# Performance work log

Measured on AMD Instinct MI355X. Metric: run time of the kernel, lower is better.

The kernel has to match this reference:

```python
import jax, jax.numpy as jnp
import numpy as np


def setup_inputs() -> dict:
    key = jax.random.key(0)
    k1, k2 = jax.random.split(key)
    B, S, F, C = 4, 1024, 512, 4   # batch, time, freq bins, in_filters
    T, K, O = 2, 4, 4              # time half-window, harmonics, out_filters
    x_in = jax.random.normal(k1, (B, S, F, C), dtype=jnp.float32)
    W = jax.random.normal(k2, (2 * T + 1, K, C, O), dtype=jnp.float32) * 0.05
    return {"x_in": x_in, "W": W}


def reference(x_in, W):
    # W: [2T+1, K, C, O]
    T = (W.shape[0] - 1) // 2
    K = W.shape[1]
    B, S, F, C = x_in.shape
    # pad time axis by T on each side (as in tf.pad in the original)
    x_pad = jnp.pad(x_in, ((0, 0), (T, T), (0, 0), (0, 0)))  # [B, S+2T, F, C]
    # harmonic index table: idx[omega, k] = (k+1) * omega, masked when out of band
    k_range = jnp.arange(1, K + 1)                 # [K]
    omega = jnp.arange(F)                          # [F]
    idx = omega[:, None] * k_range[None, :]        # [F, K]
    valid = (idx < F)                              # [F, K]
    idx_c = jnp.clip(idx, 0, F - 1)
    # vectorized harmonic gather over all (time, freq): [B, S+2T, F, K, C]
    xh = x_pad[:, :, idx_c, :] * valid[None, None, :, :, None].astype(x_pad.dtype)
    # windowed time combination: small fixed loop over 2T+1 taps avoids
    # materializing the [B, S, 2T+1, F, K, C] patch tensor
    out = jnp.zeros((B, S, F, W.shape[-1]), dtype=x_in.dtype)
    for t in range(2 * T + 1):
        out = out + jnp.einsum('bsfkc,kco->bsfo', xh[:, t:t + S], W[t])
    return out
```

## Files before the change

kernel.cpp:

```cpp
#include <hip/hip_runtime.h>


#define TS    2
#define NTAP  5
#define FB    512
#define SB    1024
#define BB    4

typedef float vfloat4 __attribute__((ext_vector_type(4)));

__device__ __forceinline__ void nt_store4(float4 v, float4* p) {
    vfloat4 raw = { v.x, v.y, v.z, v.w };
    __builtin_nontemporal_store(raw, (vfloat4*)p);
}

__global__ __launch_bounds__(256, 8)
void harmonic_conv_kernel(const float* __restrict__ x,
                          const float* __restrict__ W,
                          float* __restrict__ out) {
    const int bid  = blockIdx.x;
    const int work = ((bid & 7) << 8) + (bid >> 3);
    const int b    = work >> 9;
    const int s0   = (work & 511) * TS;
    const int tid  = threadIdx.x;

    const float4* xb = (const float4*)x + (size_t)b * SB * FB;
    float4*       ob = (float4*)out + (size_t)b * SB * FB;

    {
        const int g = tid + 256;
        float4 xw[TS + 4];
#pragma unroll
        for (int r = 0; r < TS + 4; ++r) {
            const int sp = s0 + r - 2;
            xw[r] = (sp >= 0 && sp < SB) ? xb[(size_t)sp * FB + g]
                                         : make_float4(0.f, 0.f, 0.f, 0.f);
        }
        float4 acc[TS];
#pragma unroll
        for (int j = 0; j < TS; ++j) acc[j] = make_float4(0.f, 0.f, 0.f, 0.f);
#pragma unroll
        for (int t = 0; t < NTAP; ++t) {
            const float* wp = W + t * 64;
            float w[16];
#pragma unroll
            for (int i = 0; i < 16; ++i) w[i] = wp[i];
#pragma unroll
            for (int j = 0; j < TS; ++j) {
                const float4 xv = xw[j + t];
                acc[j].x += xv.x*w[0] + xv.y*w[4] + xv.z*w[8]  + xv.w*w[12];
                acc[j].y += xv.x*w[1] + xv.y*w[5] + xv.z*w[9]  + xv.w*w[13];
                acc[j].z += xv.x*w[2] + xv.y*w[6] + xv.z*w[10] + xv.w*w[14];
                acc[j].w += xv.x*w[3] + xv.y*w[7] + xv.z*w[11] + xv.w*w[15];
            }
        }
#pragma unroll
        for (int j = 0; j < TS; ++j)
            nt_store4(acc[j], &ob[(size_t)(s0 + j) * FB + g]);
    }

    {
        const int f = tid;
        float4 acc[TS];
#pragma unroll
        for (int j = 0; j < TS; ++j) acc[j] = make_float4(0.f, 0.f, 0.f, 0.f);

#pragma unroll
        for (int m = 1; m <= 4; ++m) {
            const int g = f * m;
            if (g < FB) {
                float4 xw[TS + 4];
#pragma unroll
                for (int r = 0; r < TS + 4; ++r) {
                    const int sp = s0 + r - 2;
                    xw[r] = (sp >= 0 && sp < SB) ? xb[(size_t)sp * FB + g]
                                                 : make_float4(0.f, 0.f, 0.f, 0.f);
                }
#pragma unroll
                for (int t = 0; t < NTAP; ++t) {
                    const float* wp = W + t * 64 + (m - 1) * 16;
                    float w[16];
#pragma unroll
                    for (int i = 0; i < 16; ++i) w[i] = wp[i];
#pragma unroll
                    for (int j = 0; j < TS; ++j) {
                        const float4 xv = xw[j + t];
                        acc[j].x += xv.x*w[0] + xv.y*w[4] + xv.z*w[8]  + xv.w*w[12];
                        acc[j].y += xv.x*w[1] + xv.y*w[5] + xv.z*w[9]  + xv.w*w[13];
                        acc[j].z += xv.x*w[2] + xv.y*w[6] + xv.z*w[10] + xv.w*w[14];
                        acc[j].w += xv.x*w[3] + xv.y*w[7] + xv.z*w[11] + xv.w*w[15];
                    }
                }
            }
        }
#pragma unroll
        for (int j = 0; j < TS; ++j)
            nt_store4(acc[j], &ob[(size_t)(s0 + j) * FB + f]);
    }
}

extern "C" void kernel_launch(void* const* d_in, const int* in_sizes, int n_in,
                              void* d_out, int out_size, void* d_ws, size_t ws_size,
                              hipStream_t stream) {
    const float* x = (const float*)d_in[0];
    const float* W = (const float*)d_in[1];
    float* out = (float*)d_out;
    const int nblocks = BB * (SB / TS);
    harmonic_conv_kernel<<<nblocks, 256, 0, stream>>>(x, W, out);
}
```

Before: 95.90 us.

## Stage input time window in LDS with swizzled padding for harmonic gathers

Each block now loads its 6-row by 512-bin input window cooperatively into shared memory (about 52KB, padded and swizzled against bank conflicts), then does all harmonic gathers from LDS instead of global memory. Strided harmonic reads (f*2, f*3, f*4) previously went to global or L2 uncoalesced. Launch bounds drop from 8 to 3 blocks per CU to match the LDS footprint. In exchange the kernel pays a barrier and lower occupancy, so there is less latency hiding.

```diff
diff --git a/kernel.cpp b/kernel.cpp
--- a/kernel.cpp
+++ b/kernel.cpp
@@ -6,6 +6,8 @@
 #define FB    512
 #define SB    1024
 #define BB    4
+#define NROW  (TS + 4)
+#define ROWP  544
 
 typedef float vfloat4 __attribute__((ext_vector_type(4)));
 
@@ -14,12 +16,39 @@
     __builtin_nontemporal_store(raw, (vfloat4*)p);
 }
 
-__global__ __launch_bounds__(256, 8)
+__device__ __forceinline__ int swz(int f) { return f + (f >> 4); }
+
+__device__ __forceinline__ void accum_harm(const float4* lx, int g,
+                                           const float* __restrict__ Wk,
+                                           float4 acc[TS]) {
+    float4 xw[NROW];
+#pragma unroll
+    for (int r = 0; r < NROW; ++r) xw[r] = lx[r * ROWP + swz(g)];
+#pragma unroll
+    for (int t = 0; t < NTAP; ++t) {
+        const float* wp = Wk + t * 64;
+        float w[16];
+#pragma unroll
+        for (int i = 0; i < 16; ++i) w[i] = wp[i];
+#pragma unroll
+        for (int j = 0; j < TS; ++j) {
+            const float4 xv = xw[j + t];
+            acc[j].x += xv.x*w[0] + xv.y*w[4] + xv.z*w[8]  + xv.w*w[12];
+            acc[j].y += xv.x*w[1] + xv.y*w[5] + xv.z*w[9]  + xv.w*w[13];
+            acc[j].z += xv.x*w[2] + xv.y*w[6] + xv.z*w[10] + xv.w*w[14];
+            acc[j].w += xv.x*w[3] + xv.y*w[7] + xv.z*w[11] + xv.w*w[15];
+        }
+    }
+}
+
+__global__ __launch_bounds__(256, 3)
 void harmonic_conv_kernel(const float* __restrict__ x,
                           const float* __restrict__ W,
                           float* __restrict__ out) {
+    __shared__ float4 lx[NROW * ROWP];
+
     const int bid  = blockIdx.x;
-    const int work = ((bid & 7) << 8) + (bid >> 3);
+    const int work = ((bid & 7) << 8) | (bid >> 3);
     const int b    = work >> 9;
     const int s0   = (work & 511) * TS;
     const int tid  = threadIdx.x;
@@ -27,76 +56,36 @@
     const float4* xb = (const float4*)x + (size_t)b * SB * FB;
     float4*       ob = (float4*)out + (size_t)b * SB * FB;
 
-    {
-        const int g = tid + 256;
-        float4 xw[TS + 4];
 #pragma unroll
-        for (int r = 0; r < TS + 4; ++r) {
-            const int sp = s0 + r - 2;
-            xw[r] = (sp >= 0 && sp < SB) ? xb[(size_t)sp * FB + g]
-                                         : make_float4(0.f, 0.f, 0.f, 0.f);
-        }
-        float4 acc[TS];
-#pragma unroll
-        for (int j = 0; j < TS; ++j) acc[j] = make_float4(0.f, 0.f, 0.f, 0.f);
-#pragma unroll
-        for (int t = 0; t < NTAP; ++t) {
-            const float* wp = W + t * 64;
-            float w[16];
-#pragma unroll
-            for (int i = 0; i < 16; ++i) w[i] = wp[i];
-#pragma unroll
-            for (int j = 0; j < TS; ++j) {
-                const float4 xv = xw[j + t];
-                acc[j].x += xv.x*w[0] + xv.y*w[4] + xv.z*w[8]  + xv.w*w[12];
-                acc[j].y += xv.x*w[1] + xv.y*w[5] + xv.z*w[9]  + xv.w*w[13];
-                acc[j].z += xv.x*w[2] + xv.y*w[6] + xv.z*w[10] + xv.w*w[14];
-                acc[j].w += xv.x*w[3] + xv.y*w[7] + xv.z*w[11] + xv.w*w[15];
-            }
-        }
-#pragma unroll
-        for (int j = 0; j < TS; ++j)
-            nt_store4(acc[j], &ob[(size_t)(s0 + j) * FB + g]);
+    for (int i = 0; i < NROW * FB / 256; ++i) {
+        const int n  = i * 256 + tid;
+        const int r  = n >> 9;
+        const int f  = n & (FB - 1);
+        const int sp = s0 + r - 2;
+        float4 v = make_float4(0.f, 0.f, 0.f, 0.f);
+        if (sp >= 0 && sp < SB) v = xb[(size_t)sp * FB + f];
+        lx[r * ROWP + swz(f)] = v;
     }
+    __syncthreads();
 
-    {
-        const int f = tid;
-        float4 acc[TS];
-#pragma unroll
-        for (int j = 0; j < TS; ++j) acc[j] = make_float4(0.f, 0.f, 0.f, 0.f);
+    float4 acc[TS];
 
 #pragma unroll
-        for (int m = 1; m <= 4; ++m) {
-            const int g = f * m;
-            if (g < FB) {
-                float4 xw[TS + 4];
+    for (int j = 0; j < TS; ++j) acc[j] = make_float4(0.f, 0.f, 0.f, 0.f);
+    accum_harm(lx, tid + 256, W, acc);
 #pragma unroll
-                for (int r = 0; r < TS + 4; ++r) {
-                    const int sp = s0 + r - 2;
-                    xw[r] = (sp >= 0 && sp < SB) ? xb[(size_t)sp * FB + g]
-                                                 : make_float4(0.f, 0.f, 0.f, 0.f);
-                }
+    for (int j = 0; j < TS; ++j)
+        nt_store4(acc[j], &ob[(size_t)(s0 + j) * FB + (tid + 256)]);
+
 #pragma unroll
-                for (int t = 0; t < NTAP; ++t) {
-                    const float* wp = W + t * 64 + (m - 1) * 16;
-                    float w[16];
+    for (int j = 0; j < TS; ++j) acc[j] = make_float4(0.f, 0.f, 0.f, 0.f);
+    accum_harm(lx, tid,     W,      acc);
+    accum_harm(lx, tid * 2, W + 16, acc);
+    if (tid * 3 < FB) accum_harm(lx, tid * 3, W + 32, acc);
+    if (tid * 4 < FB) accum_harm(lx, tid * 4, W + 48, acc);
 #pragma unroll
-                    for (int i = 0; i < 16; ++i) w[i] = wp[i];
-#pragma unroll
-                    for (int j = 0; j < TS; ++j) {
-                        const float4 xv = xw[j + t];
-                        acc[j].x += xv.x*w[0] + xv.y*w[4] + xv.z*w[8]  + xv.w*w[12];
-                        acc[j].y += xv.x*w[1] + xv.y*w[5] + xv.z*w[9]  + xv.w*w[13];
-                        acc[j].z += xv.x*w[2] + xv.y*w[6] + xv.z*w[10] + xv.w*w[14];
-                        acc[j].w += xv.x*w[3] + xv.y*w[7] + xv.z*w[11] + xv.w*w[15];
-                    }
-                }
-            }
-        }
-#pragma unroll
-        for (int j = 0; j < TS; ++j)
-            nt_store4(acc[j], &ob[(size_t)(s0 + j) * FB + f]);
-    }
+    for (int j = 0; j < TS; ++j)
+        nt_store4(acc[j], &ob[(size_t)(s0 + j) * FB + tid]);
 }
 
 extern "C" void kernel_launch(void* const* d_in, const int* in_sizes, int n_in,
```

Result: no change. 94.93 us (-1.0%).
